# Kernel optimization log

Measured on AMD Instinct MI355X. Metric: run time of the kernel, lower is better.

The kernel has to match this reference:

```python
import jax, jax.numpy as jnp
import numpy as np

N = 50000      # nodes
E = 800000     # edges (before self-loops)
H = 4          # heads
C = 64         # hidden channels per head
CLS = 10       # len(bins)+1
D_IN = 64      # input feature dim
NEG_SLOPE = 0.2


def setup_inputs() -> dict:
    key = jax.random.key(0)
    ks = jax.random.split(key, 24)
    inp = {
        "x": jax.random.normal(ks[0], (N, D_IN), jnp.float32),
        "edge_index": jax.random.randint(ks[1], (2, E), 0, N),
    }
    dims = [(D_IN, C), (H * C, C), (H * C, C), (H * C, C), (H * C, CLS)]
    k = 2
    for l, (din, dout) in enumerate(dims):
        sc = 1.0 / np.sqrt(din)
        inp[f"W{l}"] = jax.random.normal(ks[k], (din, H * dout), jnp.float32) * sc; k += 1
        inp[f"as{l}"] = jax.random.normal(ks[k], (H, dout), jnp.float32) * sc; k += 1
        inp[f"ad{l}"] = jax.random.normal(ks[k], (H, dout), jnp.float32) * sc; k += 1
        inp[f"b{l}"] = jnp.zeros((H * dout,), jnp.float32)
    return inp


def gat_layer(x, src, dst, W, a_s, a_d, b):
    # PyG GATConv (concat=True): h = x W -> [N,H,Ch]
    Hh, Ch = a_s.shape
    h = (x @ W).reshape(-1, Hh, Ch)
    asn = (h * a_s).sum(-1)                      # [N,H]
    adn = (h * a_d).sum(-1)                      # [N,H]
    e = jax.nn.leaky_relu(asn[src] + adn[dst], NEG_SLOPE)   # [Et,H]
    m = jax.ops.segment_max(e, dst, num_segments=N)         # softmax over in-edges per dst
    ex = jnp.exp(e - m[dst])
    s = jax.ops.segment_sum(ex, dst, num_segments=N)
    alpha = ex / (s[dst] + 1e-16)                # [Et,H]
    out = jax.ops.segment_sum(alpha[:, :, None] * h[src], dst, num_segments=N)
    return out.reshape(-1, Hh * Ch) + b


def reference(x, edge_index, W0, as0, ad0, b0, W1, as1, ad1, b1,
              W2, as2, ad2, b2, W3, as3, ad3, b3, W4, as4, ad4, b4):
    loop = jnp.arange(N, dtype=edge_index.dtype)  # GATConv add_self_loops=True
    src = jnp.concatenate([edge_index[0], loop])
    dst = jnp.concatenate([edge_index[1], loop])
    params = [(W0, as0, ad0, b0), (W1, as1, ad1, b1), (W2, as2, ad2, b2),
              (W3, as3, ad3, b3), (W4, as4, ad4, b4)]
    for W, a_s, a_d, b in params:
        x = jax.nn.relu(gat_layer(x, src, dst, W, a_s, a_d, b))
        # dropout(p=0.5) is identity in eval mode (training=False)
    return x
```

## Files before the change

kernel.cpp:

```cpp
#include <hip/hip_runtime.h>
#include <hip/hip_bf16.h>
#include <math.h>

#define N_NODES 50000
#define N_PAD   50048
#define N_EDGES 800000
#define HEADS 4

typedef __attribute__((ext_vector_type(8))) _Float16 half8_t;
typedef __attribute__((ext_vector_type(4))) _Float16 half4_t;
typedef __attribute__((ext_vector_type(4))) float f32x4;

__device__ inline void split2(float v, _Float16& p0, _Float16& p1) {
    p0 = (_Float16)v;
    p1 = (_Float16)(v - (float)p0);
}


__global__ void init_deg_kernel(int* __restrict__ deg) {
    int i = blockIdx.x * blockDim.x + threadIdx.x;
    if (i < N_NODES) deg[i] = 1;
}

__global__ void hist_kernel(const int* __restrict__ dst, int* __restrict__ deg) {
    int i = blockIdx.x * blockDim.x + threadIdx.x;
    if (i < N_EDGES) atomicAdd(&deg[dst[i]], 1);
}

__global__ __launch_bounds__(1024) void scan_kernel(const int* __restrict__ deg,
                                                    int* __restrict__ rowptr,
                                                    int* __restrict__ cursor) {
    __shared__ int wsums[16];
    const int t = threadIdx.x;
    const int wv = t >> 6, ln = t & 63;
    const int WCHUNK = (N_NODES + 15) / 16;
    const int base = wv * WCHUNK;
    int lim = base + WCHUNK; if (lim > N_NODES) lim = N_NODES;

    int tot = 0;
    for (int i = base + ln; i < lim; i += 64) tot += deg[i];
#pragma unroll
    for (int o = 1; o < 64; o <<= 1) tot += __shfl_xor(tot, o);
    if (ln == 0) wsums[wv] = tot;
    __syncthreads();

    int run = 0;
    for (int w = 0; w < wv; ++w) run += wsums[w];

    for (int i0 = base; i0 < lim; i0 += 64) {
        int i = i0 + ln;
        int d = (i < lim) ? deg[i] : 0;
        int sc = d;
#pragma unroll
        for (int o = 1; o < 64; o <<= 1) {
            int v = __shfl_up(sc, o);
            if (ln >= o) sc += v;
        }
        if (i < lim) {
            int val = run + sc - d;
            rowptr[i] = val;
            cursor[i] = val;
        }
        run += __shfl(sc, 63);
    }
    if (t == 1023) rowptr[N_NODES] = run;
}

__global__ void scatter_kernel(const int* __restrict__ src, const int* __restrict__ dst,
                               int* __restrict__ cursor, int* __restrict__ col) {
    int i = blockIdx.x * blockDim.x + threadIdx.x;
    if (i < N_EDGES) {
        int d = dst[i];
        int pos = atomicAdd(&cursor[d], 1);
        col[pos] = src[i];
    } else if (i < N_EDGES + N_NODES) {
        int n = i - N_EDGES;
        int pos = atomicAdd(&cursor[n], 1);
        col[pos] = n;
    }
}


__global__ void x_split_kernel(const float* __restrict__ x, _Float16* __restrict__ pl,
                               size_t pstride) {
    int i = blockIdx.x * blockDim.x + threadIdx.x;
    if (i >= N_NODES * 64) return;
    _Float16 a, b;
    split2(x[i], a, b);
    pl[i] = a;
    pl[pstride + i] = b;
}

__global__ void w_split_kernel(const float* __restrict__ W, _Float16* __restrict__ wt,
                               int K, int NC) {
    int t = blockIdx.x * blockDim.x + threadIdx.x;
    int c = t >> 8, k = t & 255;
    float v = (k < K && c < NC) ? W[k * NC + c] : 0.f;
    _Float16 a, b;
    split2(v, a, b);
    wt[t] = a;
    wt[65536 + t] = b;
}


template <int FUSE_ATTN>
__global__ __launch_bounds__(256) void gemm_mfma_kernel(
        const _Float16* __restrict__ Apl, size_t apstride, int lda,
        const _Float16* __restrict__ Wt,
        _Float16* __restrict__ hpl, size_t hstride,
        float* __restrict__ C, int K, int NC,
        const float* __restrict__ as_flat, const float* __restrict__ ad_flat,
        float* __restrict__ asn, float* __restrict__ adn) {
    __shared__ _Float16 As[2][128][40];
    __shared__ _Float16 Bs[2][128][40];

    const int tid = threadIdx.x;
    const int lane = tid & 63;
    const int wave = tid >> 6;
    const int wr = (wave >> 1) * 64;
    const int wc = (wave & 1) * 64;
    const int m0 = blockIdx.x * 128;
    const int n0 = blockIdx.y * 128;

    f32x4 acc[4][4];
#pragma unroll
    for (int i = 0; i < 4; ++i)
#pragma unroll
        for (int j = 0; j < 4; ++j) acc[i][j] = (f32x4){0.f, 0.f, 0.f, 0.f};

    const int row0 = tid >> 2, q = tid & 3;
    const int row1 = row0 + 64;

    const _Float16* aptr0 = Apl + (size_t)(m0 + row0) * lda + q * 8;
    const _Float16* aptr1 = Apl + (size_t)(m0 + row1) * lda + q * 8;
    const _Float16* bptr0 = Wt + (size_t)(n0 + row0) * 256 + q * 8;
    const _Float16* bptr1 = Wt + (size_t)(n0 + row1) * 256 + q * 8;

    half8_t pa[2][2], pb[2][2];
#pragma unroll
    for (int p = 0; p < 2; ++p) {
        pa[p][0] = *(const half8_t*)(aptr0 + p * apstride);
        pa[p][1] = *(const half8_t*)(aptr1 + p * apstride);
        pb[p][0] = *(const half8_t*)(bptr0 + p * 65536);
        pb[p][1] = *(const half8_t*)(bptr1 + p * 65536);
    }

    for (int k0 = 0; k0 < K; k0 += 32) {
        if (k0) __syncthreads();
#pragma unroll
        for (int p = 0; p < 2; ++p) {
            *(half8_t*)(&As[p][row0][q * 8]) = pa[p][0];
            *(half8_t*)(&As[p][row1][q * 8]) = pa[p][1];
            *(half8_t*)(&Bs[p][row0][q * 8]) = pb[p][0];
            *(half8_t*)(&Bs[p][row1][q * 8]) = pb[p][1];
        }
        __syncthreads();

        if (k0 + 32 < K) {
            int kn = k0 + 32;
#pragma unroll
            for (int p = 0; p < 2; ++p) {
                pa[p][0] = *(const half8_t*)(aptr0 + p * apstride + kn);
                pa[p][1] = *(const half8_t*)(aptr1 + p * apstride + kn);
                pb[p][0] = *(const half8_t*)(bptr0 + p * 65536 + kn);
                pb[p][1] = *(const half8_t*)(bptr1 + p * 65536 + kn);
            }
        }

        half8_t bf[2][4];
#pragma unroll
        for (int p = 0; p < 2; ++p)
#pragma unroll
            for (int j = 0; j < 4; ++j)
                bf[p][j] = *(const half8_t*)(&Bs[p][wc + j * 16 + (lane & 15)][(lane >> 4) * 8]);

#pragma unroll
        for (int i = 0; i < 4; ++i) {
            half8_t af0 = *(const half8_t*)(&As[0][wr + i * 16 + (lane & 15)][(lane >> 4) * 8]);
            half8_t af1 = *(const half8_t*)(&As[1][wr + i * 16 + (lane & 15)][(lane >> 4) * 8]);
#pragma unroll
            for (int j = 0; j < 4; ++j) {
                f32x4 c = acc[i][j];
                c = __builtin_amdgcn_mfma_f32_16x16x32_f16(af0, bf[1][j], c, 0, 0, 0);
                c = __builtin_amdgcn_mfma_f32_16x16x32_f16(af1, bf[0][j], c, 0, 0, 0);
                c = __builtin_amdgcn_mfma_f32_16x16x32_f16(af0, bf[0][j], c, 0, 0, 0);
                acc[i][j] = c;
            }
        }
    }

    const int rbase = m0 + wr + (lane >> 4) * 4;
    const int cbase = n0 + wc + (lane & 15);

    if (FUSE_ATTN) {
#pragma unroll
        for (int i = 0; i < 4; ++i)
#pragma unroll
            for (int j = 0; j < 4; ++j) {
                int gcol = cbase + j * 16;
#pragma unroll
                for (int r4 = 0; r4 < 4; ++r4) {
                    int grow = rbase + i * 16 + r4;
                    if (grow < N_NODES) {
                        _Float16 a, b;
                        split2(acc[i][j][r4], a, b);
                        size_t off = (size_t)grow * 256 + gcol;
                        hpl[off] = a;
                        hpl[hstride + off] = b;
                    }
                }
            }
        const int hd_out = (n0 + wc) >> 6;
        float as_v[4], ad_v[4];
#pragma unroll
        for (int j = 0; j < 4; ++j) {
            int gc = cbase + j * 16;
            as_v[j] = as_flat[gc];
            ad_v[j] = ad_flat[gc];
        }
#pragma unroll
        for (int i = 0; i < 4; ++i)
#pragma unroll
            for (int r4 = 0; r4 < 4; ++r4) {
                float ps = 0.f, pd = 0.f;
#pragma unroll
                for (int j = 0; j < 4; ++j) {
                    float v = acc[i][j][r4];
                    ps += v * as_v[j];
                    pd += v * ad_v[j];
                }
#pragma unroll
                for (int o = 1; o < 16; o <<= 1) {
                    ps += __shfl_xor(ps, o);
                    pd += __shfl_xor(pd, o);
                }
                if ((lane & 15) == 0) {
                    int grow = rbase + i * 16 + r4;
                    if (grow < N_NODES) {
                        asn[grow * 4 + hd_out] = ps;
                        adn[grow * 4 + hd_out] = pd;
                    }
                }
            }
    } else {
#pragma unroll
        for (int i = 0; i < 4; ++i)
#pragma unroll
            for (int j = 0; j < 4; ++j) {
                int gcol = cbase + j * 16;
                if (gcol >= NC) continue;
#pragma unroll
                for (int r4 = 0; r4 < 4; ++r4) {
                    int grow = rbase + i * 16 + r4;
                    if (grow < N_NODES) C[(size_t)grow * NC + gcol] = acc[i][j][r4];
                }
            }
    }
}


__global__ void attn_coef_kernel(const float* __restrict__ h,
                                 const float* __restrict__ a_s,
                                 const float* __restrict__ a_d,
                                 float* __restrict__ asn, float* __restrict__ adn,
                                 int CH) {
    int t = blockIdx.x * blockDim.x + threadIdx.x;
    if (t >= N_NODES * HEADS) return;
    int n = t >> 2;
    int hd = t & 3;
    const float* hp = h + (size_t)n * HEADS * CH + hd * CH;
    const float* sp = a_s + hd * CH;
    const float* dp = a_d + hd * CH;
    float s1 = 0.f, s2 = 0.f;
    for (int c = 0; c < CH; c += 2) {
        float2 hv = *reinterpret_cast<const float2*>(&hp[c]);
        float2 av = *reinterpret_cast<const float2*>(&sp[c]);
        float2 dv = *reinterpret_cast<const float2*>(&dp[c]);
        s1 += hv.x * av.x + hv.y * av.y;
        s2 += hv.x * dv.x + hv.y * dv.y;
    }
    asn[t] = s1;
    adn[t] = s2;
}


__global__ __launch_bounds__(256) void aggregate64_kernel(
        const _Float16* __restrict__ hpl, size_t hstride,
        const float* __restrict__ asn, const float* __restrict__ adn,
        const int* __restrict__ rowptr, const int* __restrict__ col,
        const float* __restrict__ bias,
        _Float16* __restrict__ pl, size_t pstride) {
    const int n = (blockIdx.x << 2) + (threadIdx.x >> 6);
    const int lane = threadIdx.x & 63;
    const int hd = lane >> 4;
    const int e16 = lane & 15;
    const int pbase = lane & 48;

    const int start = rowptr[n];
    const int end = rowptr[n + 1];
    const float adv = adn[(n << 2) | hd];

    float m = -INFINITY, s = 0.f;
    float a0 = 0.f, a1 = 0.f, a2 = 0.f, a3 = 0.f;

    for (int e0 = start; e0 < end; e0 += 16) {
        int e = e0 + e16;
        int srcl = n;
        float ev = -INFINITY;
        if (e < end) {
            srcl = col[e];
            float t = asn[(srcl << 2) | hd] + adv;
            ev = (t > 0.f) ? t : 0.2f * t;
        }
        float bm = ev;
#pragma unroll
        for (int o = 1; o < 16; o <<= 1) bm = fmaxf(bm, __shfl_xor(bm, o));
        float mn = fmaxf(m, bm);
        float scale = __expf(m - mn);
        float p = __expf(ev - mn);
        float ps = p;
#pragma unroll
        for (int o = 1; o < 16; o <<= 1) ps += __shfl_xor(ps, o);
        s = s * scale + ps;
        a0 *= scale; a1 *= scale; a2 *= scale; a3 *= scale;
        m = mn;

        int cnt = end - e0; if (cnt > 16) cnt = 16;
        int cnt4 = (cnt + 3) & ~3;
        for (int j0 = 0; j0 < cnt4; j0 += 4) {
            int sj[4]; float pj[4];
#pragma unroll
            for (int j = 0; j < 4; ++j) {
                sj[j] = __shfl(srcl, j0 + j);
                pj[j] = __shfl(p, pbase + j0 + j);
            }
            half4_t h0[4], h1[4];
#pragma unroll
            for (int j = 0; j < 4; ++j) {
                const _Float16* hp = hpl + (size_t)sj[j] * 256 + (lane << 2);
                h0[j] = *(const half4_t*)hp;
                h1[j] = *(const half4_t*)(hp + hstride);
            }
#pragma unroll
            for (int j = 0; j < 4; ++j) {
                a0 += pj[j] * ((float)h0[j][0] + (float)h1[j][0]);
                a1 += pj[j] * ((float)h0[j][1] + (float)h1[j][1]);
                a2 += pj[j] * ((float)h0[j][2] + (float)h1[j][2]);
                a3 += pj[j] * ((float)h0[j][3] + (float)h1[j][3]);
            }
        }
    }

    float sd = s + 1e-16f;
    const float* bp = bias + (lane << 2);
    float v0 = fmaxf(a0 / sd + bp[0], 0.f);
    float v1 = fmaxf(a1 / sd + bp[1], 0.f);
    float v2 = fmaxf(a2 / sd + bp[2], 0.f);
    float v3 = fmaxf(a3 / sd + bp[3], 0.f);

    _Float16 s0a, s0b, s1a, s1b, s2a, s2b, s3a, s3b;
    split2(v0, s0a, s0b);
    split2(v1, s1a, s1b);
    split2(v2, s2a, s2b);
    split2(v3, s3a, s3b);
    half4_t o0, o1;
    o0[0] = s0a; o0[1] = s1a; o0[2] = s2a; o0[3] = s3a;
    o1[0] = s0b; o1[1] = s1b; o1[2] = s2b; o1[3] = s3b;
    size_t off = (size_t)n * 256 + (lane << 2);
    *(half4_t*)(pl + off) = o0;
    *(half4_t*)(pl + pstride + off) = o1;
}


template <int CH>
__global__ __launch_bounds__(256) void aggregate_out_kernel(
        const float* __restrict__ h, const float* __restrict__ asn,
        const float* __restrict__ adn, const int* __restrict__ rowptr,
        const int* __restrict__ col, const float* __restrict__ bias,
        float* __restrict__ out) {
    constexpr int HC = HEADS * CH;
    __shared__ float2 pair_lds[HEADS][32];

    const int n = blockIdx.x;
    const int hd = threadIdx.x >> 6;
    const int lane = threadIdx.x & 63;
    const int el = lane & 31;
    const int hdoff = hd * CH + lane;

    const int start = rowptr[n];
    const int end = rowptr[n + 1];
    const float adv = adn[(n << 2) | hd];

    float m = -INFINITY, s = 0.f;
    float accv[4] = {0.f, 0.f, 0.f, 0.f};

    for (int e0 = start; e0 < end; e0 += 32) {
        int e = e0 + el;
        bool valid = (lane < 32) && (e < end);
        int srcl = n;
        float ev = -INFINITY;
        if (valid) {
            srcl = col[e];
            float t = asn[(srcl << 2) | hd] + adv;
            ev = (t > 0.f) ? t : 0.2f * t;
        }
        float bm = ev;
#pragma unroll
        for (int o = 1; o < 64; o <<= 1) bm = fmaxf(bm, __shfl_xor(bm, o));
        float mn = fmaxf(m, bm);
        float scale = __expf(m - mn);
        float p = __expf(ev - mn);
        float ps = p;
#pragma unroll
        for (int o = 1; o < 64; o <<= 1) ps += __shfl_xor(ps, o);
        s = s * scale + ps;
#pragma unroll
        for (int c = 0; c < 4; ++c) accv[c] *= scale;
        m = mn;

        if (lane < 32) pair_lds[hd][lane] = make_float2(__int_as_float(srcl), p);

        int cnt = end - e0; if (cnt > 32) cnt = 32;
        int cnt8 = (cnt + 7) & ~7;
        for (int i0 = 0; i0 < cnt8; i0 += 8) {
            int sv[8]; float pv[8];
#pragma unroll
            for (int j = 0; j < 8; ++j) {
                float2 pr = pair_lds[hd][i0 + j];
                sv[j] = __float_as_int(pr.x);
                pv[j] = pr.y;
            }
            float hv[8];
#pragma unroll
            for (int j = 0; j < 8; ++j)
                hv[j] = (lane < CH) ? h[(size_t)sv[j] * HC + hdoff] : 0.f;
#pragma unroll
            for (int j = 0; j < 8; ++j) accv[j & 3] += pv[j] * hv[j];
        }
    }

    if (lane < CH) {
        float acc = (accv[0] + accv[1]) + (accv[2] + accv[3]);
        float v = acc / (s + 1e-16f) + bias[hd * CH + lane];
        out[n * HC + hd * CH + lane] = fmaxf(v, 0.f);
    }
}


extern "C" void kernel_launch(void* const* d_in, const int* in_sizes, int n_in,
                              void* d_out, int out_size, void* d_ws, size_t ws_size,
                              hipStream_t stream) {
    const float* x_in = (const float*)d_in[0];
    const int* ei = (const int*)d_in[1];
    const int* src = ei;
    const int* dst = ei + N_EDGES;

    const float *W[5], *AS[5], *AD[5], *BI[5];
    for (int l = 0; l < 5; ++l) {
        W[l]  = (const float*)d_in[2 + l * 4 + 0];
        AS[l] = (const float*)d_in[2 + l * 4 + 1];
        AD[l] = (const float*)d_in[2 + l * 4 + 2];
        BI[l] = (const float*)d_in[2 + l * 4 + 3];
    }

    const size_t PSTRIDE = (size_t)N_PAD * 256;
    _Float16* planes = (_Float16*)d_ws;
    _Float16* hpl = planes + 2 * PSTRIDE;
    float* Hb   = (float*)(hpl + 2 * PSTRIDE);
    float* asn  = Hb + (size_t)N_NODES * 40;
    float* adn  = asn + (size_t)N_NODES * HEADS;
    int* rowptr = (int*)(adn + (size_t)N_NODES * HEADS);
    int* cursor = rowptr + (N_NODES + 1);
    int* col    = cursor + N_NODES;
    _Float16* wt = (_Float16*)(((uintptr_t)(col + N_EDGES + N_NODES) + 15) & ~(uintptr_t)15);

    init_deg_kernel<<<(N_NODES + 255) / 256, 256, 0, stream>>>(cursor);
    hist_kernel<<<(N_EDGES + 255) / 256, 256, 0, stream>>>(dst, cursor);
    scan_kernel<<<1, 1024, 0, stream>>>(cursor, rowptr, cursor);
    scatter_kernel<<<(N_EDGES + N_NODES + 255) / 256, 256, 0, stream>>>(src, dst, cursor, col);

    for (int l = 0; l < 5; ++l) {
        int Kl = (l == 0) ? 64 : 256;
        int NCl = (l == 4) ? 40 : 256;
        w_split_kernel<<<256, 256, 0, stream>>>(W[l], wt + (size_t)l * 2 * 65536, Kl, NCl);
    }
    x_split_kernel<<<(N_NODES * 64 + 255) / 256, 256, 0, stream>>>(x_in, planes, PSTRIDE);

    int lda = 64;
    for (int l = 0; l < 5; ++l) {
        const int K = (l == 0) ? 64 : 256;
        const int NC = (l == 4) ? 40 : 256;
        dim3 ggrid(N_PAD / 128, (NC + 127) / 128);
        const _Float16* wl = wt + (size_t)l * 2 * 65536;
        if (l < 4) {
            gemm_mfma_kernel<1><<<ggrid, 256, 0, stream>>>(
                planes, PSTRIDE, lda, wl, hpl, PSTRIDE, nullptr, K, NC,
                AS[l], AD[l], asn, adn);
            aggregate64_kernel<<<N_NODES / 4, 256, 0, stream>>>(
                hpl, PSTRIDE, asn, adn, rowptr, col, BI[l], planes, PSTRIDE);
        } else {
            gemm_mfma_kernel<0><<<ggrid, 256, 0, stream>>>(
                planes, PSTRIDE, lda, wl, nullptr, 0, Hb, K, NC,
                AS[l], AD[l], asn, adn);
            attn_coef_kernel<<<(N_NODES * HEADS + 255) / 256, 256, 0, stream>>>(
                Hb, AS[l], AD[l], asn, adn, 10);
            aggregate_out_kernel<10><<<N_NODES, 256, 0, stream>>>(
                Hb, asn, adn, rowptr, col, BI[l], (float*)d_out);
        }
        lda = 256;
    }
    (void)in_sizes; (void)n_in; (void)out_size; (void)ws_size;
}
```

Baseline: 933.3 us.

## Use direct global-to-LDS loads with k-tiled swizzled operand layout in GEMM

Activation and weight half-precision planes are stored in a k-tile-major, XOR-swizzled layout (32-wide k slabs per row), produced by the split kernels and the aggregation epilogue. The GEMM then fills shared memory with global_load_lds DMA instead of register-staged loads followed by LDS stores, and reads fragments using the matching swizzle to avoid bank conflicts. This removes register prefetching and padded LDS, but also drops the software double-buffering overlap of the next tile's loads with compute.

```diff
diff --git a/kernel.cpp b/kernel.cpp
--- a/kernel.cpp
+++ b/kernel.cpp
@@ -15,6 +15,7 @@
     p0 = (_Float16)v;
     p1 = (_Float16)(v - (float)p0);
 }
+
 
 
 __global__ void init_deg_kernel(int* __restrict__ deg) {
@@ -85,10 +86,13 @@
                                size_t pstride) {
     int i = blockIdx.x * blockDim.x + threadIdx.x;
     if (i >= N_NODES * 64) return;
+    int n = i >> 6, k = i & 63;
     _Float16 a, b;
     split2(x[i], a, b);
-    pl[i] = a;
-    pl[pstride + i] = b;
+    size_t off = (size_t)(k >> 5) * ((size_t)N_PAD * 32) + (size_t)n * 32 +
+                 ((((k >> 3) & 3) ^ (n & 3)) << 3) + (k & 7);
+    pl[off] = a;
+    pl[pstride + off] = b;
 }
 
 __global__ void w_split_kernel(const float* __restrict__ W, _Float16* __restrict__ wt,
@@ -98,21 +102,22 @@
     float v = (k < K && c < NC) ? W[k * NC + c] : 0.f;
     _Float16 a, b;
     split2(v, a, b);
-    wt[t] = a;
-    wt[65536 + t] = b;
+    size_t off = (size_t)(k >> 5) * 8192 + (size_t)c * 32 +
+                 ((((k >> 3) & 3) ^ (c & 3)) << 3) + (k & 7);
+    wt[off] = a;
+    wt[65536 + off] = b;
 }
 
 
 template <int FUSE_ATTN>
 __global__ __launch_bounds__(256) void gemm_mfma_kernel(
-        const _Float16* __restrict__ Apl, size_t apstride, int lda,
+        const _Float16* __restrict__ Apl, size_t apstride,
         const _Float16* __restrict__ Wt,
         _Float16* __restrict__ hpl, size_t hstride,
         float* __restrict__ C, int K, int NC,
         const float* __restrict__ as_flat, const float* __restrict__ ad_flat,
         float* __restrict__ asn, float* __restrict__ adn) {
-    __shared__ _Float16 As[2][128][40];
-    __shared__ _Float16 Bs[2][128][40];
+    __shared__ __align__(16) _Float16 lds[16384];
 
     const int tid = threadIdx.x;
     const int lane = tid & 63;
@@ -128,56 +133,57 @@
 #pragma unroll
         for (int j = 0; j < 4; ++j) acc[i][j] = (f32x4){0.f, 0.f, 0.f, 0.f};
 
-    const int row0 = tid >> 2, q = tid & 3;
-    const int row1 = row0 + 64;
-
-    const _Float16* aptr0 = Apl + (size_t)(m0 + row0) * lda + q * 8;
-    const _Float16* aptr1 = Apl + (size_t)(m0 + row1) * lda + q * 8;
-    const _Float16* bptr0 = Wt + (size_t)(n0 + row0) * 256 + q * 8;
-    const _Float16* bptr1 = Wt + (size_t)(n0 + row1) * 256 + q * 8;
-
-    half8_t pa[2][2], pb[2][2];
-#pragma unroll
-    for (int p = 0; p < 2; ++p) {
-        pa[p][0] = *(const half8_t*)(aptr0 + p * apstride);
-        pa[p][1] = *(const half8_t*)(aptr1 + p * apstride);
-        pb[p][0] = *(const half8_t*)(bptr0 + p * 65536);
-        pb[p][1] = *(const half8_t*)(bptr1 + p * 65536);
-    }
-
-    for (int k0 = 0; k0 < K; k0 += 32) {
-        if (k0) __syncthreads();
-#pragma unroll
-        for (int p = 0; p < 2; ++p) {
-            *(half8_t*)(&As[p][row0][q * 8]) = pa[p][0];
-            *(half8_t*)(&As[p][row1][q * 8]) = pa[p][1];
-            *(half8_t*)(&Bs[p][row0][q * 8]) = pb[p][0];
-            *(half8_t*)(&Bs[p][row1][q * 8]) = pb[p][1];
+    const _Float16* gptr[8];
+    size_t ktstep;
+    {
+        const _Float16* sbase;
+        int rowbase;
+        if (wave < 2) {
+            sbase = Apl + (size_t)wave * apstride;
+            rowbase = m0;
+            ktstep = (size_t)N_PAD * 32;
+        } else {
+            sbase = Wt + (size_t)(wave - 2) * 65536;
+            rowbase = n0;
+            ktstep = 8192;
+        }
+#pragma unroll
+        for (int it = 0; it < 8; ++it) {
+            int idx = it * 64 + lane;
+            gptr[it] = sbase + (size_t)(rowbase + (idx >> 2)) * 32 + (idx & 3) * 8;
+        }
+    }
+    char* ldsw = (char*)lds + wave * 8192;
+
+    const int cswz = ((lane >> 4) ^ (lane & 3)) << 3;
+    const _Float16* Ab = lds;
+    const _Float16* Bb = lds + 8192;
+
+    const int KT = K >> 5;
+    for (int kt = 0; kt < KT; ++kt) {
+        if (kt) __syncthreads();
+#pragma unroll
+        for (int it = 0; it < 8; ++it) {
+            __builtin_amdgcn_global_load_lds(
+                (const __attribute__((address_space(1))) void*)(gptr[it] + kt * ktstep),
+                (__attribute__((address_space(3))) void*)(ldsw + it * 1024),
+                16, 0, 0);
         }
         __syncthreads();
 
-        if (k0 + 32 < K) {
-            int kn = k0 + 32;
-#pragma unroll
-            for (int p = 0; p < 2; ++p) {
-                pa[p][0] = *(const half8_t*)(aptr0 + p * apstride + kn);
-                pa[p][1] = *(const half8_t*)(aptr1 + p * apstride + kn);
-                pb[p][0] = *(const half8_t*)(bptr0 + p * 65536 + kn);
-                pb[p][1] = *(const half8_t*)(bptr1 + p * 65536 + kn);
-            }
-        }
-
         half8_t bf[2][4];
 #pragma unroll
         for (int p = 0; p < 2; ++p)
 #pragma unroll
-            for (int j = 0; j < 4; ++j)
-                bf[p][j] = *(const half8_t*)(&Bs[p][wc + j * 16 + (lane & 15)][(lane >> 4) * 8]);
-
+            for (int j = 0; j < 4; ++j) {
+                int r = wc + j * 16 + (lane & 15);
+                bf[p][j] = *(const half8_t*)(Bb + p * 4096 + r * 32 + cswz);
+            }
 #pragma unroll
         for (int i = 0; i < 4; ++i) {
-            half8_t af0 = *(const half8_t*)(&As[0][wr + i * 16 + (lane & 15)][(lane >> 4) * 8]);
-            half8_t af1 = *(const half8_t*)(&As[1][wr + i * 16 + (lane & 15)][(lane >> 4) * 8]);
+            int r = wr + i * 16 + (lane & 15);
+            half8_t af0 = *(const half8_t*)(Ab + r * 32 + cswz);
+            half8_t af1 = *(const half8_t*)(Ab + 4096 + r * 32 + cswz);
 #pragma unroll
             for (int j = 0; j < 4; ++j) {
                 f32x4 c = acc[i][j];
@@ -366,7 +372,11 @@
     half4_t o0, o1;
     o0[0] = s0a; o0[1] = s1a; o0[2] = s2a; o0[3] = s3a;
     o1[0] = s0b; o1[1] = s1b; o1[2] = s2b; o1[3] = s3b;
-    size_t off = (size_t)n * 256 + (lane << 2);
+
+    const int kt = lane >> 3;
+    const int cp = ((lane >> 1) & 3) ^ (n & 3);
+    const int inner = (lane & 1) << 2;
+    size_t off = (size_t)kt * ((size_t)N_PAD * 32) + (size_t)n * 32 + (cp << 3) + inner;
     *(half4_t*)(pl + off) = o0;
     *(half4_t*)(pl + pstride + off) = o1;
 }
@@ -486,7 +496,6 @@
     }
     x_split_kernel<<<(N_NODES * 64 + 255) / 256, 256, 0, stream>>>(x_in, planes, PSTRIDE);
 
-    int lda = 64;
     for (int l = 0; l < 5; ++l) {
         const int K = (l == 0) ? 64 : 256;
         const int NC = (l == 4) ? 40 : 256;
@@ -494,20 +503,19 @@
         const _Float16* wl = wt + (size_t)l * 2 * 65536;
         if (l < 4) {
             gemm_mfma_kernel<1><<<ggrid, 256, 0, stream>>>(
-                planes, PSTRIDE, lda, wl, hpl, PSTRIDE, nullptr, K, NC,
+                planes, PSTRIDE, wl, hpl, PSTRIDE, nullptr, K, NC,
                 AS[l], AD[l], asn, adn);
             aggregate64_kernel<<<N_NODES / 4, 256, 0, stream>>>(
                 hpl, PSTRIDE, asn, adn, rowptr, col, BI[l], planes, PSTRIDE);
         } else {
             gemm_mfma_kernel<0><<<ggrid, 256, 0, stream>>>(
-                planes, PSTRIDE, lda, wl, nullptr, 0, Hb, K, NC,
+                planes, PSTRIDE, wl, nullptr, 0, Hb, K, NC,
                 AS[l], AD[l], asn, adn);
             attn_coef_kernel<<<(N_NODES * HEADS + 255) / 256, 256, 0, stream>>>(
                 Hb, AS[l], AD[l], asn, adn, 10);
             aggregate_out_kernel<10><<<N_NODES, 256, 0, stream>>>(
                 Hb, asn, adn, rowptr, col, BI[l], (float*)d_out);
         }
-        lda = 256;
     }
     (void)in_sizes; (void)n_in; (void)out_size; (void)ws_size;
 }
```

New measurement: 927.6 us. Within noise of the previous version (-0.6%).
